# Kernel optimization log

Hardware: AMD Instinct MI355X
Metric: run time of the kernel (lower is better)

Reference implementation:

```python
import jax, jax.numpy as jnp
import numpy as np

NB_CLS, NB_QRY, NB_SHOT, FEAT_DIM = 5, 75, 5, 640
Q_STEPS, LR_DNI, HID = 3, 1e-3, 4096
N = NB_CLS + NB_QRY           # nodes in similarity graph (80)
M = 1 + N                     # subgraph size (81)
# strict upper triangle of MxM minus the query-query block (matches triu_index_input)
_t = np.ones((M, M)); _t[1 + NB_CLS:, 1 + NB_CLS:] = 0
_t = np.triu(_t, 1)
MASK_IDX = jnp.asarray(np.flatnonzero(_t.ravel() == 1))
DNI_IN = int(MASK_IDX.shape[0])  # 465


def _pairwise(supp, query):
    feat = jnp.concatenate([supp, query], 0)
    nrm = jnp.maximum(jnp.linalg.norm(feat, axis=-1, keepdims=True), 1e-12)
    feat = feat / nrm
    sim = feat @ feat.T                      # (N, N)
    sim_ss = sim[:NB_CLS, :NB_CLS]
    sim_qq = sim[NB_CLS:, NB_CLS:]
    sim_sq = sim[:NB_CLS, NB_CLS:]
    sim_feat_support = jnp.concatenate([sim_ss, sim_sq], 1).T   # (N, nb_cls)
    sim_feat_query = jnp.concatenate([sim_sq, sim_qq], 0)       # (N, nb_qry)
    return sim_feat_support, sim_feat_query, sim_sq


def _subgraph(sim_s, sim_q):
    # topk indices are constants wrt grad (no_grad in torch; ints in jax)
    idx_q = jax.lax.top_k(sim_q, NB_QRY)[1] + NB_CLS
    idx_s = jax.lax.top_k(sim_s, NB_CLS)[1]
    index = jnp.concatenate([jnp.arange(N, dtype=idx_s.dtype)[:, None], idx_s, idx_q], 1)  # (N, M)
    sim = jnp.concatenate([sim_s, sim_q], 1)                     # (N, N)
    sub = sim[index[:, :, None], index[:, None, :]]              # (N, M, M) batched gather
    return sub.reshape(N, M * M)[:, MASK_IDX]                    # (N, DNI_IN)


def _dni(x, W1, b1, W2, b2, W3, b3):
    h = jax.nn.relu(x @ W1.T + b1)
    h = jax.nn.relu(h @ W2.T + b2)
    return h @ W3.T + b3


def _refine(supp, query, ds, dq):
    for _ in range(Q_STEPS):
        inputs, vjp = jax.vjp(lambda s: _subgraph(*_pairwise(s, query)[:2]), supp)
        supp = supp - LR_DNI * vjp(_dni(inputs, *ds))[0]
        inputs, vjp = jax.vjp(lambda q: _subgraph(*_pairwise(supp, q)[:2]), query)
        query = query - LR_DNI * vjp(_dni(inputs, *dq))[0]
    return supp, query


def setup_inputs() -> dict:
    key = jax.random.key(0)
    ks = jax.random.split(key, 16)
    d = {
        "feat_support": jax.random.normal(ks[0], (NB_CLS, NB_SHOT, FEAT_DIM), jnp.float32),
        "feat_query": jax.random.normal(ks[1], (NB_QRY, FEAT_DIM), jnp.float32),
        "scale_cls": jnp.full((1,), 10.0, jnp.float32),
    }
    names = ["ds_W1", "ds_b1", "ds_W2", "ds_b2", "ds_W3", "ds_b3",
             "dq_W1", "dq_b1", "dq_W2", "dq_b2", "dq_W3", "dq_b3"]
    shapes = [(HID, DNI_IN), (HID,), (HID, HID), (HID,), (DNI_IN, HID), (DNI_IN,)] * 2
    for i, (n, sh) in enumerate(zip(names, shapes)):
        d[n] = jax.random.normal(ks[2 + i], sh, jnp.float32) * 0.02
    return d


def reference(feat_support, feat_query, scale_cls,
              ds_W1, ds_b1, ds_W2, ds_b2, ds_W3, ds_b3,
              dq_W1, dq_b1, dq_W2, dq_b2, dq_W3, dq_b3):
    supp = feat_support.mean(1)                                  # (nb_cls, feat_dim)
    ds = (ds_W1, ds_b1, ds_W2, ds_b2, ds_W3, ds_b3)
    dq = (dq_W1, dq_b1, dq_W2, dq_b2, dq_W3, dq_b3)
    supp, query = _refine(supp, feat_query, ds, dq)
    _, _, sim_sq = _pairwise(supp, query)
    return (sim_sq * scale_cls).T                                # (nb_qry, nb_cls)
```

## Files before the change

### kernel.cpp

```cpp
#include <hip/hip_runtime.h>

#define NCLS 5
#define NQRY 75
#define NTOT 80
#define FD   640
#define HIDN 4096
#define DNIN 465
#define KPAD 512
#define NPAD 512
#define LRDNI 1e-3f

#define KS1 4
#define KS2 8
#define KS3 32

typedef short  v8s __attribute__((ext_vector_type(8)));
typedef float  v4f __attribute__((ext_vector_type(4)));

__device__ __forceinline__ ushort f2bf(float x) {
    uint u = __float_as_uint(x);
    u = (u + 0x7FFFu + ((u >> 16) & 1u)) >> 16;
    return (ushort)u;
}
__device__ __forceinline__ uint pk2(float a, float b) {
    return (uint)f2bf(a) | ((uint)f2bf(b) << 16);
}

__global__ __launch_bounds__(256) void k_setup(
                        const float* __restrict__ fs, const float* __restrict__ fq,
                        const float* __restrict__ W1s, const float* __restrict__ W1q,
                        const float* __restrict__ W2s, const float* __restrict__ W2q,
                        const float* __restrict__ W3s, const float* __restrict__ W3q,
                        ushort* __restrict__ W1bs, ushort* __restrict__ W1bq,
                        ushort* __restrict__ W2bs, ushort* __restrict__ W2bq,
                        ushort* __restrict__ W3bs, ushort* __restrict__ W3bq,
                        float* __restrict__ supp, float* __restrict__ qbuf) {
    int tid = blockIdx.x * 256 + threadIdx.x;

    #pragma unroll
    for (int i = 0; i < 4; i++) {
        int oo = tid + i * 524288;
        int l = oo & 63, ks = (oo >> 6) & 127, nt = oo >> 13;
        int n = nt * 16 + (l & 15), kb = ks * 32 + ((l >> 4) << 3);
        size_t src = (size_t)n * HIDN + kb;
        float4 s0 = *(const float4*)(W2s + src);
        float4 s1 = *(const float4*)(W2s + src + 4);
        float4 t0 = *(const float4*)(W2q + src);
        float4 t1 = *(const float4*)(W2q + src + 4);
        uint4 qa, qb;
        qa.x = pk2(s0.x, s0.y); qa.y = pk2(s0.z, s0.w);
        qa.z = pk2(s1.x, s1.y); qa.w = pk2(s1.z, s1.w);
        qb.x = pk2(t0.x, t0.y); qb.y = pk2(t0.z, t0.w);
        qb.z = pk2(t1.x, t1.y); qb.w = pk2(t1.z, t1.w);
        *(uint4*)(W2bs + (size_t)oo * 8) = qa;
        *(uint4*)(W2bq + (size_t)oo * 8) = qb;
    }

    {
        int oo = tid & 262143;
        const float* Ws = (tid < 262144) ? W1s : W1q;
        ushort* Wd = (tid < 262144) ? W1bs : W1bq;
        int l = oo & 63, ks = (oo >> 6) & 15, nt = oo >> 10;
        int n = nt * 16 + (l & 15), kb = ks * 32 + ((l >> 4) << 3);
        ushort tmp[8];
        #pragma unroll
        for (int j = 0; j < 8; j++) {
            int k = kb + j;
            tmp[j] = (k < DNIN) ? f2bf(Ws[n * DNIN + k]) : (ushort)0;
        }
        *(uint4*)(Wd + (size_t)oo * 8) = *(uint4*)tmp;
    }

    {
        int oo = tid & 262143;
        const float* Ws = (tid < 262144) ? W3s : W3q;
        ushort* Wd = (tid < 262144) ? W3bs : W3bq;
        int l = oo & 63, ks = (oo >> 6) & 127, nt = oo >> 13;
        int n = nt * 16 + (l & 15), kb = ks * 32 + ((l >> 4) << 3);
        uint4 q;
        if (n < DNIN) {
            float4 f0 = *(const float4*)(Ws + (size_t)n * HIDN + kb);
            float4 f1 = *(const float4*)(Ws + (size_t)n * HIDN + kb + 4);
            q.x = pk2(f0.x, f0.y); q.y = pk2(f0.z, f0.w);
            q.z = pk2(f1.x, f1.y); q.w = pk2(f1.z, f1.w);
        } else q = (uint4){0, 0, 0, 0};
        *(uint4*)(Wd + (size_t)oo * 8) = q;
    }

    if (tid < NCLS * FD) {
        int c = tid / FD, d = tid % FD;
        float s = 0.f;
        #pragma unroll
        for (int t = 0; t < 5; t++) s += fs[(c * 5 + t) * FD + d];
        supp[tid] = s * 0.2f;
    }
    if (tid < NQRY * FD / 4)
        ((float4*)qbuf)[tid] = ((const float4*)fq)[tid];
}

__device__ __forceinline__ const float* rowptr(const float* supp, const float* qbuf, int r) {
    return (r < NCLS) ? (supp + r * FD) : (qbuf + (r - NCLS) * FD);
}

template<bool FIN>
__global__ void k_simrank(const float* __restrict__ supp, const float* __restrict__ qbuf,
                          float* __restrict__ f, float* __restrict__ nrm,
                          float* __restrict__ S, int* __restrict__ perm,
                          const float* __restrict__ scale, float* __restrict__ out) {
    __shared__ float fi[FD];
    __shared__ float row[NTOT];
    __shared__ float ssh[NTOT];
    int i = blockIdx.x;
    int t = threadIdx.x;
    const float* ri = rowptr(supp, qbuf, i);
    for (int u = t; u < FD; u += 128) fi[u] = ri[u];
    __syncthreads();
    float dot = 0.f;
    if (t < NTOT) {
        const float* rj = rowptr(supp, qbuf, t);
        float ss = 0.f;
        for (int k = 0; k < FD; k += 4) {
            float4 a = *(const float4*)(fi + k);
            float4 b = *(const float4*)(rj + k);
            dot += a.x * b.x + a.y * b.y + a.z * b.z + a.w * b.w;
            ss  += b.x * b.x + b.y * b.y + b.z * b.z + b.w * b.w;
        }
        ssh[t] = ss;
    }
    __syncthreads();
    float ni = fmaxf(sqrtf(ssh[i]), 1e-12f);
    float inv_i = 1.0f / ni;
    if (t < NTOT) {
        float nt = fmaxf(sqrtf(ssh[t]), 1e-12f);
        float val = dot * inv_i / nt;
        if (FIN) {
            if (t >= NCLS) out[(t - NCLS) * NCLS + i] = val * scale[0];
        } else {
            row[t] = val;
            S[i * NTOT + t] = val;
        }
    }
    if (FIN) return;
    __syncthreads();
    for (int u = t; u < FD; u += 128) f[i * FD + u] = fi[u] * inv_i;
    if (t == 0) { nrm[i] = ni; perm[i * 81] = i; }
    if (t < NCLS) {
        float v = row[t]; int rank = 0;
        for (int k = 0; k < NCLS; k++) {
            float w = row[k];
            if (w > v || (w == v && k < t)) rank++;
        }
        perm[i * 81 + 1 + rank] = t;
    } else if (t < NTOT) {
        int j = t - NCLS; float v = row[t]; int rank = 0;
        for (int k = NCLS; k < NTOT; k++) {
            float w = row[k];
            if (w > v || (w == v && (k - NCLS) < j)) rank++;
        }
        perm[i * 81 + 6 + rank] = t;
    }
}

__device__ __forceinline__ void mask_ab(int m, int& a, int& b) {
    int start = 0, len = 80, aa = 0;
    while (m >= start + len) { start += len; len--; aa++; }
    a = aa; b = aa + 1 + (m - start);
}

__global__ void k_gather(const float* __restrict__ S, const int* __restrict__ perm,
                         ushort* __restrict__ Xb, float* __restrict__ Gs) {
    __shared__ int p[81];
    int i = blockIdx.x;
    int t = threadIdx.x;
    if (t < 81) p[t] = perm[i * 81 + t];
    if (t < NTOT) Gs[i * NTOT + t] = 0.f;
    __syncthreads();
    if (t < DNIN) {
        int a, b; mask_ab(t, a, b);
        Xb[i * KPAD + t] = f2bf(S[p[a] * NTOT + p[b]]);
    } else if (t < KPAD) {
        Xb[i * KPAD + t] = 0;
    }
}

template<int NT, int KSTEPS>
__global__ __launch_bounds__(256) void k_gemm(
        const ushort* __restrict__ A, int lda,
        const ushort* __restrict__ Bf, int nks,
        float* __restrict__ C, int ldc) {
    int tid = threadIdx.x;
    int w = tid >> 6, lane = tid & 63, l16 = lane & 15, quad = lane >> 4;
    int n0 = blockIdx.x * (NT * 64) + w * NT * 16;
    int kc0 = blockIdx.y * (KSTEPS * 32);
    const ushort* Ap = A + l16 * lda + kc0 + quad * 8;
    const ushort* Bp = Bf + ((size_t)(n0 >> 4) * nks + (kc0 >> 5)) * 512 + lane * 8;

    v4f acc[5][NT];
    #pragma unroll
    for (int mt = 0; mt < 5; mt++)
        #pragma unroll
        for (int nt = 0; nt < NT; nt++) acc[mt][nt] = (v4f){0.f, 0.f, 0.f, 0.f};

    #pragma unroll
    for (int s = 0; s < KSTEPS; s++) {
        v8s a[5], b[NT];
        #pragma unroll
        for (int mt = 0; mt < 5; mt++)
            a[mt] = *(const v8s*)(Ap + mt * 16 * lda + s * 32);
        #pragma unroll
        for (int nt = 0; nt < NT; nt++)
            b[nt] = *(const v8s*)(Bp + ((size_t)nt * nks + s) * 512);
        #pragma unroll
        for (int mt = 0; mt < 5; mt++)
            #pragma unroll
            for (int nt = 0; nt < NT; nt++)
                acc[mt][nt] = __builtin_amdgcn_mfma_f32_16x16x32_bf16(a[mt], b[nt], acc[mt][nt], 0, 0, 0);
    }
    float* Cp = C + (size_t)blockIdx.y * 80 * ldc;
    #pragma unroll
    for (int nt = 0; nt < NT; nt++) {
        int col = n0 + nt * 16 + l16;
        #pragma unroll
        for (int mt = 0; mt < 5; mt++)
            #pragma unroll
            for (int r = 0; r < 4; r++)
                Cp[(mt * 16 + quad * 4 + r) * ldc + col] = acc[mt][nt][r];
    }
}

template<int NS>
__global__ void k_ep(const float* __restrict__ P, const float* __restrict__ bias,
                     ushort* __restrict__ H) {
    int idx = blockIdx.x * 256 + threadIdx.x;
    float4 s = ((const float4*)bias)[idx & 1023];
    #pragma unroll
    for (int ks = 0; ks < NS; ks++) {
        float4 p = ((const float4*)P)[ks * (80 * HIDN / 4) + idx];
        s.x += p.x; s.y += p.y; s.z += p.z; s.w += p.w;
    }
    uint2 q;
    q.x = pk2(fmaxf(s.x, 0.f), fmaxf(s.y, 0.f));
    q.y = pk2(fmaxf(s.z, 0.f), fmaxf(s.w, 0.f));
    ((uint2*)H)[idx] = q;
}

__global__ void k_scatter(const float* __restrict__ P3, const float* __restrict__ b3,
                          const int* __restrict__ perm, float* __restrict__ Gs) {
    __shared__ int p[81];
    int i = blockIdx.x;
    int t = threadIdx.x;
    if (t < 81) p[t] = perm[i * 81 + t];
    __syncthreads();
    if (t < DNIN) {
        float g = b3[t];
        #pragma unroll
        for (int ks = 0; ks < KS3; ks++) g += P3[ks * (80 * NPAD) + i * NPAD + t];
        int a, b; mask_ab(t, a, b);
        atomicAdd(&Gs[p[a] * NTOT + p[b]], g);
    }
}

__global__ void k_bwd(const float* __restrict__ Gs, const float* __restrict__ f,
                      const float* __restrict__ nrm, float* __restrict__ target,
                      int row0) {
    int r = row0 + blockIdx.x;
    __shared__ float cj[NTOT];
    __shared__ float red[2];
    int t = threadIdx.x;
    if (t < NTOT) cj[t] = Gs[r * NTOT + t] + Gs[t * NTOT + r];
    __syncthreads();
    float df[5] = {0.f, 0.f, 0.f, 0.f, 0.f};
    for (int j = 0; j < NTOT; j++) {
        float c = cj[j];
        const float* fj = f + j * FD;
        #pragma unroll
        for (int u = 0; u < 5; u++) df[u] += c * fj[t + 128 * u];
    }
    const float* fr = f + r * FD;
    float frv[5]; float partial = 0.f;
    #pragma unroll
    for (int u = 0; u < 5; u++) { frv[u] = fr[t + 128 * u]; partial += df[u] * frv[u]; }
    #pragma unroll
    for (int o = 32; o > 0; o >>= 1) partial += __shfl_xor(partial, o, 64);
    if ((t & 63) == 0) red[t >> 6] = partial;
    __syncthreads();
    float dot = red[0] + red[1];
    float invn = 1.0f / nrm[r];
    float* dst = target + blockIdx.x * FD;
    #pragma unroll
    for (int u = 0; u < 5; u++) {
        float dx = (df[u] - dot * frv[u]) * invn;
        dst[t + 128 * u] -= LRDNI * dx;
    }
}

extern "C" void kernel_launch(void* const* d_in, const int* in_sizes, int n_in,
                              void* d_out, int out_size, void* d_ws, size_t ws_size,
                              hipStream_t stream) {
    const float* fs    = (const float*)d_in[0];
    const float* fq    = (const float*)d_in[1];
    const float* scale = (const float*)d_in[2];
    const float* W[12];
    for (int i = 0; i < 12; i++) W[i] = (const float*)d_in[3 + i];

    float* base = (float*)d_ws;
    float* supp = base;
    float* qbuf = supp + 3200;
    float* f    = qbuf + 48000;
    float* nrm  = f + 51200;
    float* S    = nrm + 96;
    int*   perm = (int*)(S + 6400);
    float* P1   = (float*)(perm + 6496);
    float* P2   = P1 + (size_t)KS1 * 80 * HIDN;
    float* P3   = P2 + (size_t)KS2 * 80 * HIDN;
    float* Gs   = P3 + (size_t)KS3 * 80 * NPAD;
    ushort* Xb  = (ushort*)(Gs + 6400);
    ushort* H1b = Xb + 80 * KPAD;
    ushort* H2b = H1b + 80 * HIDN;
    ushort* W1b_ds = H2b + 80 * HIDN;
    ushort* W1b_dq = W1b_ds + HIDN * KPAD;
    ushort* W3b_ds = W1b_dq + HIDN * KPAD;
    ushort* W3b_dq = W3b_ds + NPAD * HIDN;
    ushort* W2b_ds = W3b_dq + NPAD * HIDN;
    ushort* W2b_dq = W2b_ds + (size_t)HIDN * HIDN;

    k_setup<<<2048, 256, 0, stream>>>(fs, fq, W[0], W[6], W[2], W[8], W[4], W[10],
                                      W1b_ds, W1b_dq, W2b_ds, W2b_dq, W3b_ds, W3b_dq,
                                      supp, qbuf);

    for (int step = 0; step < 3; step++) {
        for (int half = 0; half < 2; half++) {
            const float* const* w = (half == 0) ? W : (W + 6);
            const ushort* W1b = (half == 0) ? W1b_ds : W1b_dq;
            const ushort* W2b = (half == 0) ? W2b_ds : W2b_dq;
            const ushort* W3b = (half == 0) ? W3b_ds : W3b_dq;
            k_simrank<false><<<80, 128, 0, stream>>>(supp, qbuf, f, nrm, S, perm, nullptr, nullptr);
            k_gather<<<80, 512, 0, stream>>>(S, perm, Xb, Gs);
            k_gemm<1, 4><<<dim3(64, KS1), 256, 0, stream>>>(Xb, KPAD, W1b, 16, P1, HIDN);
            k_ep<KS1><<<320, 256, 0, stream>>>(P1, w[1], H1b);
            k_gemm<1, 16><<<dim3(64, KS2), 256, 0, stream>>>(H1b, HIDN, W2b, 128, P2, HIDN);
            k_ep<KS2><<<320, 256, 0, stream>>>(P2, w[3], H2b);
            k_gemm<1, 4><<<dim3(8, KS3), 256, 0, stream>>>(H2b, HIDN, W3b, 128, P3, NPAD);
            k_scatter<<<80, 512, 0, stream>>>(P3, w[5], perm, Gs);
            if (half == 0) k_bwd<<<5, 128, 0, stream>>>(Gs, f, nrm, supp, 0);
            else           k_bwd<<<75, 128, 0, stream>>>(Gs, f, nrm, qbuf, NCLS);
        }
    }
    k_simrank<true><<<5, 128, 0, stream>>>(supp, qbuf, f, nrm, S, perm, scale, (float*)d_out);
}
```

Baseline: 656.9 us.

## Stage weight conversion through LDS for coalesced reads in setup kernel

Rewrites the setup kernel that converts the fp32 DNI weights to bf16 in the MFMA-fragment layout. Each block now loads a 16-row tile with coalesced row-major float4 reads, packs it to bf16 in padded shared memory, then writes it out in the swizzled fragment order. Before, each thread gathered strided 8-element chunks straight from global memory, which gave poorly coalesced reads. The change adds shared-memory traffic and a barrier per block, and spreads W1, W2, W3 and the input copies across separate block ranges.

```diff
diff --git a/kernel.cpp b/kernel.cpp
--- a/kernel.cpp
+++ b/kernel.cpp
@@ -14,6 +14,8 @@
 #define KS2 8
 #define KS3 32
 
+#define LDW 1032
+
 typedef short  v8s __attribute__((ext_vector_type(8)));
 typedef float  v4f __attribute__((ext_vector_type(4)));
 
@@ -35,67 +37,80 @@
                         ushort* __restrict__ W2bs, ushort* __restrict__ W2bq,
                         ushort* __restrict__ W3bs, ushort* __restrict__ W3bq,
                         float* __restrict__ supp, float* __restrict__ qbuf) {
-    int tid = blockIdx.x * 256 + threadIdx.x;
-
-    #pragma unroll
-    for (int i = 0; i < 4; i++) {
-        int oo = tid + i * 524288;
-        int l = oo & 63, ks = (oo >> 6) & 127, nt = oo >> 13;
-        int n = nt * 16 + (l & 15), kb = ks * 32 + ((l >> 4) << 3);
-        size_t src = (size_t)n * HIDN + kb;
-        float4 s0 = *(const float4*)(W2s + src);
-        float4 s1 = *(const float4*)(W2s + src + 4);
-        float4 t0 = *(const float4*)(W2q + src);
-        float4 t1 = *(const float4*)(W2q + src + 4);
-        uint4 qa, qb;
-        qa.x = pk2(s0.x, s0.y); qa.y = pk2(s0.z, s0.w);
-        qa.z = pk2(s1.x, s1.y); qa.w = pk2(s1.z, s1.w);
-        qb.x = pk2(t0.x, t0.y); qb.y = pk2(t0.z, t0.w);
-        qb.z = pk2(t1.x, t1.y); qb.w = pk2(t1.z, t1.w);
-        *(uint4*)(W2bs + (size_t)oo * 8) = qa;
-        *(uint4*)(W2bq + (size_t)oo * 8) = qb;
-    }
-
-    {
-        int oo = tid & 262143;
-        const float* Ws = (tid < 262144) ? W1s : W1q;
-        ushort* Wd = (tid < 262144) ? W1bs : W1bq;
-        int l = oo & 63, ks = (oo >> 6) & 15, nt = oo >> 10;
-        int n = nt * 16 + (l & 15), kb = ks * 32 + ((l >> 4) << 3);
-        ushort tmp[8];
-        #pragma unroll
-        for (int j = 0; j < 8; j++) {
-            int k = kb + j;
-            tmp[j] = (k < DNIN) ? f2bf(Ws[n * DNIN + k]) : (ushort)0;
-        }
-        *(uint4*)(Wd + (size_t)oo * 8) = *(uint4*)tmp;
-    }
-
-    {
-        int oo = tid & 262143;
-        const float* Ws = (tid < 262144) ? W3s : W3q;
-        ushort* Wd = (tid < 262144) ? W3bs : W3bq;
-        int l = oo & 63, ks = (oo >> 6) & 127, nt = oo >> 13;
-        int n = nt * 16 + (l & 15), kb = ks * 32 + ((l >> 4) << 3);
-        uint4 q;
-        if (n < DNIN) {
-            float4 f0 = *(const float4*)(Ws + (size_t)n * HIDN + kb);
-            float4 f1 = *(const float4*)(Ws + (size_t)n * HIDN + kb + 4);
-            q.x = pk2(f0.x, f0.y); q.y = pk2(f0.z, f0.w);
-            q.z = pk2(f1.x, f1.y); q.w = pk2(f1.z, f1.w);
-        } else q = (uint4){0, 0, 0, 0};
-        *(uint4*)(Wd + (size_t)oo * 8) = q;
-    }
-
-    if (tid < NCLS * FD) {
-        int c = tid / FD, d = tid % FD;
-        float s = 0.f;
-        #pragma unroll
-        for (int t = 0; t < 5; t++) s += fs[(c * 5 + t) * FD + d];
-        supp[tid] = s * 0.2f;
-    }
-    if (tid < NQRY * FD / 4)
-        ((float4*)qbuf)[tid] = ((const float4*)fq)[tid];
+    __shared__ ushort lds[16 * LDW];
+    int t = threadIdx.x;
+    int bb = blockIdx.x;
+
+    if (bb < 2304) {
+        const float* Ws; ushort* Wd; int nt, chunk, rowlim;
+        if (bb < 2048) {
+            int mat = bb >> 10, local = bb & 1023;
+            nt = local >> 2; chunk = local & 3; rowlim = 1 << 30;
+            Ws = mat ? W2q : W2s;  Wd = mat ? W2bq : W2bs;
+        } else {
+            int tt = bb - 2048;
+            int mat = tt >> 7, local = tt & 127;
+            nt = local >> 2; chunk = local & 3; rowlim = DNIN;
+            Ws = mat ? W3q : W3s;  Wd = mat ? W3bq : W3bs;
+        }
+        int row0 = nt * 16;
+        const float* src = Ws + (size_t)row0 * HIDN + chunk * 1024;
+
+        #pragma unroll
+        for (int it = 0; it < 16; it++) {
+            int idx = it * 256 + t;
+            int r = idx >> 8, c4 = idx & 255;
+            float4 v;
+            if (row0 + r < rowlim) v = *((const float4*)(src + (size_t)r * HIDN) + c4);
+            else                   v = (float4){0.f, 0.f, 0.f, 0.f};
+            uint2 q;
+            q.x = pk2(v.x, v.y);
+            q.y = pk2(v.z, v.w);
+            *(uint2*)(lds + r * LDW + c4 * 4) = q;
+        }
+        __syncthreads();
+        ushort* dst = Wd + (size_t)((nt * 4 + chunk) * 2048) * 8;
+        #pragma unroll
+        for (int it = 0; it < 8; it++) {
+            int oct = it * 256 + t;
+            int ks = oct >> 6, l = oct & 63;
+            int nl = l & 15, kk = ks * 32 + ((l >> 4) << 3);
+            *(uint4*)(dst + (size_t)oct * 8) = *(const uint4*)(lds + nl * LDW + kk);
+        }
+    } else if (bb < 2816) {
+        int tt = bb - 2304;
+        int mat = tt >> 8, nt = tt & 255;
+        const float* Ws = mat ? W1q : W1s;
+        ushort* Wd = mat ? W1bq : W1bs;
+        int row0 = nt * 16;
+        #pragma unroll
+        for (int it = 0; it < 32; it++) {
+            int idx = it * 256 + t;
+            int r = idx >> 9, c = idx & 511;
+            float val = (c < DNIN) ? Ws[(size_t)(row0 + r) * DNIN + c] : 0.f;
+            lds[r * LDW + c] = f2bf(val);
+        }
+        __syncthreads();
+        ushort* dst = Wd + (size_t)nt * 1024 * 8;
+        #pragma unroll
+        for (int it = 0; it < 4; it++) {
+            int oct = it * 256 + t;
+            int ks = oct >> 6, l = oct & 63;
+            int nl = l & 15, kk = ks * 32 + ((l >> 4) << 3);
+            *(uint4*)(dst + (size_t)oct * 8) = *(const uint4*)(lds + nl * LDW + kk);
+        }
+    } else {
+        int tid2 = (bb - 2816) * 256 + t;
+        if (tid2 < NCLS * FD) {
+            int c = tid2 / FD, d = tid2 % FD;
+            float s = 0.f;
+            #pragma unroll
+            for (int u = 0; u < 5; u++) s += fs[(c * 5 + u) * FD + d];
+            supp[tid2] = s * 0.2f;
+        }
+        for (int i = tid2; i < NQRY * FD / 4; i += 4096)
+            ((float4*)qbuf)[i] = ((const float4*)fq)[i];
+    }
 }
 
 __device__ __forceinline__ const float* rowptr(const float* supp, const float* qbuf, int r) {
@@ -324,7 +339,7 @@
     ushort* W2b_ds = W3b_dq + NPAD * HIDN;
     ushort* W2b_dq = W2b_ds + (size_t)HIDN * HIDN;
 
-    k_setup<<<2048, 256, 0, stream>>>(fs, fq, W[0], W[6], W[2], W[8], W[4], W[10],
+    k_setup<<<2832, 256, 0, stream>>>(fs, fq, W[0], W[6], W[2], W[8], W[4], W[10],
                                       W1b_ds, W1b_dq, W2b_ds, W2b_dq, W3b_ds, W3b_dq,
                                       supp, qbuf);
 
```

New measurement: 665.6 us. About the same (+1.3%).

## Replace global split-K partials with in-block wave split-K reduction and fused epilogue

Applied to the files above, without the earlier changes.

The three DNI GEMMs used to write split-K partials to global memory and then run separate epilogue kernels that summed them and applied bias and ReLU. Each block now computes one 16-column tile, splits K across its waves, reduces the partial tiles in shared memory, and applies bias, ReLU and the bf16 store directly. This removes the partial-sum global traffic and two launches per half-step, and lets the scatter read a single P3. The cost is fewer blocks (256 or 32 instead of 256 to 512) with a long serial K loop per wave, which may reduce the parallelism available for streaming W2.

```diff
diff --git a/kernel.cpp b/kernel.cpp
--- a/kernel.cpp
+++ b/kernel.cpp
@@ -9,10 +9,6 @@
 #define KPAD 512
 #define NPAD 512
 #define LRDNI 1e-3f
-
-#define KS1 4
-#define KS2 8
-#define KS3 32
 
 typedef short  v8s __attribute__((ext_vector_type(8)));
 typedef float  v4f __attribute__((ext_vector_type(4)));
@@ -183,65 +179,57 @@
     }
 }
 
-template<int NT, int KSTEPS>
-__global__ __launch_bounds__(256) void k_gemm(
+template<int WAVES, int KPW, bool EPI>
+__global__ __launch_bounds__(WAVES * 64) void k_gemmws(
         const ushort* __restrict__ A, int lda,
         const ushort* __restrict__ Bf, int nks,
-        float* __restrict__ C, int ldc) {
-    int tid = threadIdx.x;
-    int w = tid >> 6, lane = tid & 63, l16 = lane & 15, quad = lane >> 4;
-    int n0 = blockIdx.x * (NT * 64) + w * NT * 16;
-    int kc0 = blockIdx.y * (KSTEPS * 32);
+        const float* __restrict__ bias, ushort* __restrict__ H,
+        float* __restrict__ C, int ldcp) {
+    __shared__ v4f red[WAVES][5][64];
+    int t = threadIdx.x;
+    int w = t >> 6, lane = t & 63, l16 = lane & 15, quad = lane >> 4;
+    int n0 = blockIdx.x * 16;
+    int kc0 = w * (KPW * 32);
     const ushort* Ap = A + l16 * lda + kc0 + quad * 8;
-    const ushort* Bp = Bf + ((size_t)(n0 >> 4) * nks + (kc0 >> 5)) * 512 + lane * 8;
-
-    v4f acc[5][NT];
-    #pragma unroll
-    for (int mt = 0; mt < 5; mt++)
-        #pragma unroll
-        for (int nt = 0; nt < NT; nt++) acc[mt][nt] = (v4f){0.f, 0.f, 0.f, 0.f};
-
-    #pragma unroll
-    for (int s = 0; s < KSTEPS; s++) {
-        v8s a[5], b[NT];
+    const ushort* Bp = Bf + ((size_t)blockIdx.x * nks + (kc0 >> 5)) * 512 + lane * 8;
+
+    v4f acc[5];
+    #pragma unroll
+    for (int mt = 0; mt < 5; mt++) acc[mt] = (v4f){0.f, 0.f, 0.f, 0.f};
+
+    #pragma unroll
+    for (int s = 0; s < KPW; s++) {
+        v8s a[5], b;
         #pragma unroll
         for (int mt = 0; mt < 5; mt++)
             a[mt] = *(const v8s*)(Ap + mt * 16 * lda + s * 32);
-        #pragma unroll
-        for (int nt = 0; nt < NT; nt++)
-            b[nt] = *(const v8s*)(Bp + ((size_t)nt * nks + s) * 512);
+        b = *(const v8s*)(Bp + (size_t)s * 512);
         #pragma unroll
         for (int mt = 0; mt < 5; mt++)
+            acc[mt] = __builtin_amdgcn_mfma_f32_16x16x32_bf16(a[mt], b, acc[mt], 0, 0, 0);
+    }
+    #pragma unroll
+    for (int mt = 0; mt < 5; mt++) red[w][mt][lane] = acc[mt];
+    __syncthreads();
+
+    #pragma unroll
+    for (int j = 0; j < (1280 + WAVES * 64 - 1) / (WAVES * 64); j++) {
+        int row = j * (WAVES * 4) + (t >> 4);
+        if (row < 80) {
+            int col = t & 15;
+            int mt = row >> 4, rr = row & 15, qq = rr >> 2, r = rr & 3;
+            int ln = qq * 16 + col;
+            float v = 0.f;
             #pragma unroll
-            for (int nt = 0; nt < NT; nt++)
-                acc[mt][nt] = __builtin_amdgcn_mfma_f32_16x16x32_bf16(a[mt], b[nt], acc[mt][nt], 0, 0, 0);
-    }
-    float* Cp = C + (size_t)blockIdx.y * 80 * ldc;
-    #pragma unroll
-    for (int nt = 0; nt < NT; nt++) {
-        int col = n0 + nt * 16 + l16;
-        #pragma unroll
-        for (int mt = 0; mt < 5; mt++)
-            #pragma unroll
-            for (int r = 0; r < 4; r++)
-                Cp[(mt * 16 + quad * 4 + r) * ldc + col] = acc[mt][nt][r];
-    }
-}
-
-template<int NS>
-__global__ void k_ep(const float* __restrict__ P, const float* __restrict__ bias,
-                     ushort* __restrict__ H) {
-    int idx = blockIdx.x * 256 + threadIdx.x;
-    float4 s = ((const float4*)bias)[idx & 1023];
-    #pragma unroll
-    for (int ks = 0; ks < NS; ks++) {
-        float4 p = ((const float4*)P)[ks * (80 * HIDN / 4) + idx];
-        s.x += p.x; s.y += p.y; s.z += p.z; s.w += p.w;
-    }
-    uint2 q;
-    q.x = pk2(fmaxf(s.x, 0.f), fmaxf(s.y, 0.f));
-    q.y = pk2(fmaxf(s.z, 0.f), fmaxf(s.w, 0.f));
-    ((uint2*)H)[idx] = q;
+            for (int w2 = 0; w2 < WAVES; w2++) v += red[w2][mt][ln][r];
+            if (EPI) {
+                v += bias[n0 + col];
+                H[(size_t)row * HIDN + n0 + col] = f2bf(fmaxf(v, 0.f));
+            } else {
+                C[(size_t)row * ldcp + n0 + col] = v;
+            }
+        }
+    }
 }
 
 __global__ void k_scatter(const float* __restrict__ P3, const float* __restrict__ b3,
@@ -252,9 +240,7 @@
     if (t < 81) p[t] = perm[i * 81 + t];
     __syncthreads();
     if (t < DNIN) {
-        float g = b3[t];
-        #pragma unroll
-        for (int ks = 0; ks < KS3; ks++) g += P3[ks * (80 * NPAD) + i * NPAD + t];
+        float g = b3[t] + P3[i * NPAD + t];
         int a, b; mask_ab(t, a, b);
         atomicAdd(&Gs[p[a] * NTOT + p[b]], g);
     }
@@ -310,10 +296,8 @@
     float* nrm  = f + 51200;
     float* S    = nrm + 96;
     int*   perm = (int*)(S + 6400);
-    float* P1   = (float*)(perm + 6496);
-    float* P2   = P1 + (size_t)KS1 * 80 * HIDN;
-    float* P3   = P2 + (size_t)KS2 * 80 * HIDN;
-    float* Gs   = P3 + (size_t)KS3 * 80 * NPAD;
+    float* P3   = (float*)(perm + 6496);
+    float* Gs   = P3 + 80 * NPAD;
     ushort* Xb  = (ushort*)(Gs + 6400);
     ushort* H1b = Xb + 80 * KPAD;
     ushort* H2b = H1b + 80 * HIDN;
@@ -336,11 +320,12 @@
             const ushort* W3b = (half == 0) ? W3b_ds : W3b_dq;
             k_simrank<false><<<80, 128, 0, stream>>>(supp, qbuf, f, nrm, S, perm, nullptr, nullptr);
             k_gather<<<80, 512, 0, stream>>>(S, perm, Xb, Gs);
-            k_gemm<1, 4><<<dim3(64, KS1), 256, 0, stream>>>(Xb, KPAD, W1b, 16, P1, HIDN);
-            k_ep<KS1><<<320, 256, 0, stream>>>(P1, w[1], H1b);
-            k_gemm<1, 16><<<dim3(64, KS2), 256, 0, stream>>>(H1b, HIDN, W2b, 128, P2, HIDN);
-            k_ep<KS2><<<320, 256, 0, stream>>>(P2, w[3], H2b);
-            k_gemm<1, 4><<<dim3(8, KS3), 256, 0, stream>>>(H2b, HIDN, W3b, 128, P3, NPAD);
+            k_gemmws<4, 4, true><<<256, 256, 0, stream>>>(
+                Xb, KPAD, W1b, 16, w[1], H1b, nullptr, 0);
+            k_gemmws<4, 32, true><<<256, 256, 0, stream>>>(
+                H1b, HIDN, W2b, 128, w[3], H2b, nullptr, 0);
+            k_gemmws<8, 16, false><<<32, 512, 0, stream>>>(
+                H2b, HIDN, W3b, 128, nullptr, nullptr, P3, NPAD);
             k_scatter<<<80, 512, 0, stream>>>(P3, w[5], perm, Gs);
             if (half == 0) k_bwd<<<5, 128, 0, stream>>>(Gs, f, nrm, supp, 0);
             else           k_bwd<<<75, 128, 0, stream>>>(Gs, f, nrm, qbuf, NCLS);
```

Result: slower. 731.8 us (+11.4%).
